# Kernel tuning notes

Measured on AMD Instinct MI355X. Metric: run time of the kernel, lower is better.

## Reference

```python
import jax, jax.numpy as jnp
import numpy as np

E, HEADS, HD, L, FF = 768, 12, 64, 12, 3072


def layernorm(x, g, b, eps=1e-5):
    m = jnp.mean(x, axis=-1, keepdims=True)
    v = jnp.var(x, axis=-1, keepdims=True)
    return (x - m) / jnp.sqrt(v + eps) * g + b


def setup_inputs() -> dict:
    key = jax.random.key(0)
    ks = jax.random.split(key, 26)
    B, N, PS = 32, 1024, 24
    P2 = PS * PS
    def rn(k, shape, s=0.02):
        return jax.random.normal(k, shape, dtype=jnp.float32) * s
    return {
        "scene_masks": jax.random.normal(ks[0], (B, N, PS, PS), dtype=jnp.float32),
        "target_mask": jax.random.normal(ks[1], (B, PS, PS), dtype=jnp.float32),
        "emb_W": rn(ks[2], (E, P2)),            # torch Linear weight [out,in]
        "emb_b": rn(ks[3], (E,)),
        "class_embed": rn(ks[4], (1, 1, E)),
        "scene_pos": rn(ks[5], (1, N + 1, E)),
        "target_pos": rn(ks[6], (1, 2, E)),
        "ln1_g": jnp.ones((L, E), jnp.float32),
        "ln1_b": jnp.zeros((L, E), jnp.float32),
        "ln2_g": jnp.ones((L, E), jnp.float32),
        "ln2_b": jnp.zeros((L, E), jnp.float32),
        "Wq": rn(ks[7], (L, HD, HD)),
        "Wk": rn(ks[8], (L, HD, HD)),
        "Wv": rn(ks[9], (L, HD, HD)),
        "Wo": rn(ks[10], (L, E, E)),
        "bo": rn(ks[11], (L, E)),
        "W1": rn(ks[12], (L, FF, E)),
        "b1": rn(ks[13], (L, FF)),
        "W2": rn(ks[14], (L, E, FF)),
        "b2": rn(ks[15], (L, E)),
        "mlp_W": rn(ks[16], (N, E)),
        "mlp_b": rn(ks[17], (N,)),
    }


def _forward_logits(scene_masks, target_mask, emb_W, emb_b, class_embed, scene_pos,
                    target_pos, ln1_g, ln1_b, ln2_g, ln2_b, Wq, Wk, Wv, Wo, bo,
                    W1, b1, W2, b2, mlp_W, mlp_b):
    B, N, H, W = scene_masks.shape
    P2 = H * W
    scene = scene_masks.reshape(B, N, P2) @ emb_W.T + emb_b          # [B,N,E]
    tgt = target_mask.reshape(B, 1, P2) @ emb_W.T + emb_b            # [B,1,E]
    cls = jnp.broadcast_to(class_embed, (B, 1, E))
    scene = jnp.concatenate([cls, scene], axis=1) + scene_pos[:, :N + 1]  # [B,N+1,E]
    tgt = jnp.concatenate([cls, tgt], axis=1) + target_pos               # [B,2,E]
    scale = jnp.sqrt(jnp.float32(E))

    def block(tq, p):
        g1, bb1n, g2, bb2n, wq, wk, wv, wo, bo_, w1, b1_, w2, b2_ = p
        kv = layernorm(scene, g1, bb1n)                # norm1(value)=norm1(key)
        q = layernorm(tq, g1, bb1n)                    # norm1(query)
        kvh = kv.reshape(B, N + 1, HEADS, HD)
        qh = q.reshape(B, 2, HEADS, HD)
        # per-head Linear shares one [HD,HD] weight across all heads
        qs = jnp.einsum('nqhd,ed->nqhe', qh, wq)
        ks_ = jnp.einsum('nkhd,ed->nkhe', kvh, wk)
        vs = jnp.einsum('nkhd,ed->nkhe', kvh, wv)
        energy = jnp.einsum('nqhd,nkhd->nhqk', qs, ks_)     # [B,H,2,N+1]
        att = jax.nn.softmax(energy / scale, axis=-1)
        out = jnp.einsum('nhqk,nkhd->nqhd', att, vs).reshape(B, 2, E)
        out = out @ wo.T + bo_
        x = layernorm(out + tq, g1, bb1n)
        ff = jax.nn.relu(x @ w1.T + b1_) @ w2.T + b2_
        return layernorm(ff + x, g2, bb2n), None

    params = (ln1_g, ln1_b, ln2_g, ln2_b, Wq, Wk, Wv, Wo, bo, W1, b1, W2, b2)
    tgt, _ = jax.lax.scan(block, tgt, params)
    x = jnp.mean(tgt, axis=1) @ mlp_W.T + mlp_b       # [B, num_patches]
    return x


def reference(scene_masks, target_mask, emb_W, emb_b, class_embed, scene_pos,
              target_pos, ln1_g, ln1_b, ln2_g, ln2_b, Wq, Wk, Wv, Wo, bo,
              W1, b1, W2, b2, mlp_W, mlp_b):
    x = _forward_logits(scene_masks, target_mask, emb_W, emb_b, class_embed,
                        scene_pos, target_pos, ln1_g, ln1_b, ln2_g, ln2_b,
                        Wq, Wk, Wv, Wo, bo, W1, b1, W2, b2, mlp_W, mlp_b)
    # sorted_nodes = argsort desc + 1; eye(P+1)[nodes-1] == one_hot(argsort desc)
    order = jnp.argsort(-x, axis=1)[:, :5]                # top-5 patch indices
    return jax.nn.one_hot(order, x.shape[1] + 1, dtype=jnp.float32)  # [B,5,P+1]
```

## Files before the change

kernel.cpp:

```cpp
#include <hip/hip_runtime.h>
#include <math.h>

#define E_DIM 768
#define NTOK 1025
#define B_DIM 32
#define NHEADS 12
#define HDIM 64
#define LAYERS 12
#define FF_DIM 3072
#define P2 576

__device__ __forceinline__ float block_reduce_sum(float v, float* red) {
  int tid = threadIdx.x;
  red[tid] = v;
  __syncthreads();
#pragma unroll
  for (int s = 128; s > 0; s >>= 1) {
    if (tid < s) red[tid] += red[tid + s];
    __syncthreads();
  }
  float r = red[0];
  __syncthreads();
  return r;
}

__global__ __launch_bounds__(256) void embed_gemm(
    const float* __restrict__ A, const float* __restrict__ W,
    const float* __restrict__ bias, const float* __restrict__ pos,
    float* __restrict__ scene) {
  __shared__ float Xs[16][132];
  __shared__ float Ws[16][132];
  int tid = threadIdx.x;
  int n0 = blockIdx.x * 128;
  int m0 = blockIdx.y * 128;
  int lr = tid >> 2;
  int lk = (tid & 3) << 2;
  int ty = tid >> 4, tx = tid & 15;
  float acc[8][8] = {};
  for (int k0 = 0; k0 < P2; k0 += 16) {
    float4 x0 = *(const float4*)(A + (size_t)(m0 + lr) * P2 + k0 + lk);
    float4 x1 = *(const float4*)(A + (size_t)(m0 + 64 + lr) * P2 + k0 + lk);
    float4 w0 = *(const float4*)(W + (size_t)(n0 + lr) * P2 + k0 + lk);
    float4 w1 = *(const float4*)(W + (size_t)(n0 + 64 + lr) * P2 + k0 + lk);
    __syncthreads();
    Xs[lk + 0][lr] = x0.x; Xs[lk + 1][lr] = x0.y; Xs[lk + 2][lr] = x0.z; Xs[lk + 3][lr] = x0.w;
    Xs[lk + 0][64 + lr] = x1.x; Xs[lk + 1][64 + lr] = x1.y; Xs[lk + 2][64 + lr] = x1.z; Xs[lk + 3][64 + lr] = x1.w;
    Ws[lk + 0][lr] = w0.x; Ws[lk + 1][lr] = w0.y; Ws[lk + 2][lr] = w0.z; Ws[lk + 3][lr] = w0.w;
    Ws[lk + 0][64 + lr] = w1.x; Ws[lk + 1][64 + lr] = w1.y; Ws[lk + 2][64 + lr] = w1.z; Ws[lk + 3][64 + lr] = w1.w;
    __syncthreads();
#pragma unroll
    for (int kk = 0; kk < 16; ++kk) {
      float4 a0 = *(const float4*)&Xs[kk][ty << 2];
      float4 a1 = *(const float4*)&Xs[kk][64 + (ty << 2)];
      float4 b0 = *(const float4*)&Ws[kk][tx << 2];
      float4 b1 = *(const float4*)&Ws[kk][64 + (tx << 2)];
      float av[8] = {a0.x, a0.y, a0.z, a0.w, a1.x, a1.y, a1.z, a1.w};
      float bv[8] = {b0.x, b0.y, b0.z, b0.w, b1.x, b1.y, b1.z, b1.w};
#pragma unroll
      for (int i = 0; i < 8; ++i)
#pragma unroll
        for (int j = 0; j < 8; ++j) acc[i][j] += av[i] * bv[j];
    }
  }
#pragma unroll
  for (int i = 0; i < 8; ++i) {
    int mloc = (i < 4) ? ((ty << 2) + i) : (64 + (ty << 2) + i - 4);
    int m = m0 + mloc;
    int b = m >> 10, nt = m & 1023;
    size_t row = ((size_t)b * NTOK + 1 + nt) * E_DIM;
    size_t prow = (size_t)(1 + nt) * E_DIM;
#pragma unroll
    for (int half = 0; half < 2; ++half) {
      int n = n0 + half * 64 + (tx << 2);
      float4 o4;
      o4.x = acc[i][half * 4 + 0] + bias[n + 0] + pos[prow + n + 0];
      o4.y = acc[i][half * 4 + 1] + bias[n + 1] + pos[prow + n + 1];
      o4.z = acc[i][half * 4 + 2] + bias[n + 2] + pos[prow + n + 2];
      o4.w = acc[i][half * 4 + 3] + bias[n + 3] + pos[prow + n + 3];
      *(float4*)&scene[row + n] = o4;
    }
  }
}

__global__ void scene_cls(const float* __restrict__ cls, const float* __restrict__ pos,
                          float* __restrict__ scene) {
  int b = blockIdx.x;
  for (int e = threadIdx.x; e < E_DIM; e += 256)
    scene[(size_t)b * NTOK * E_DIM + e] = cls[e] + pos[e];
}

__global__ __launch_bounds__(256) void ln_rows(const float* __restrict__ in, float* __restrict__ out) {
  __shared__ float red[256];
  int r = blockIdx.x, tid = threadIdx.x;
  const float* x = in + (size_t)r * E_DIM;
  float a0 = x[tid], a1 = x[tid + 256], a2 = x[tid + 512];
  float mean = block_reduce_sum(a0 + a1 + a2, red) * (1.f / 768.f);
  float d0 = a0 - mean, d1 = a1 - mean, d2 = a2 - mean;
  float var = block_reduce_sum(d0 * d0 + d1 * d1 + d2 * d2, red) * (1.f / 768.f);
  float rinv = rsqrtf(var + 1e-5f);
  float* o = out + (size_t)r * E_DIM;
  o[tid] = d0 * rinv; o[tid + 256] = d1 * rinv; o[tid + 512] = d2 * rinv;
}

__global__ __launch_bounds__(256) void tgt_init(
    const float* __restrict__ tmask, const float* __restrict__ W,
    const float* __restrict__ bias, const float* __restrict__ cls,
    const float* __restrict__ tpos, float* __restrict__ tq) {
  int b = blockIdx.x, tid = threadIdx.x;
  for (int e = tid; e < E_DIM; e += 256)
    tq[(size_t)(b * 2) * E_DIM + e] = cls[e] + tpos[e];
  const float* tm = tmask + (size_t)b * P2;
  for (int e = tid; e < E_DIM; e += 256) {
    const float* wr = W + (size_t)e * P2;
    float s = 0.f;
    for (int k = 0; k < P2; k += 4) {
      float4 w4 = *(const float4*)&wr[k];
      float4 t4 = *(const float4*)&tm[k];
      s += w4.x * t4.x + w4.y * t4.y + w4.z * t4.z + w4.w * t4.w;
    }
    tq[(size_t)(b * 2 + 1) * E_DIM + e] = s + bias[e] + tpos[E_DIM + e];
  }
}

__global__ void prep_m(const float* __restrict__ Wq, const float* __restrict__ Wk,
                       float* __restrict__ Mb) {
  int l = blockIdx.y;
  int idx = blockIdx.x * 256 + threadIdx.x;
  int d = idx >> 6, dp = idx & 63;
  const float* wq = Wq + l * 4096;
  const float* wk = Wk + l * 4096;
  float s = 0.f;
#pragma unroll 8
  for (int e = 0; e < 64; ++e) s += wq[e * 64 + d] * wk[e * 64 + dp];
  Mb[l * 4096 + idx] = s;
}

__global__ void prep_wvo(const float* __restrict__ Wv, const float* __restrict__ Wo,
                         float* __restrict__ Wvo) {
  int l = blockIdx.y;
  int idx = blockIdx.x * 256 + threadIdx.x;
  int ep = idx / 768, hd = idx % 768;
  int h = hd >> 6, d = hd & 63;
  const float* wv = Wv + (size_t)l * 4096;
  const float* wo = Wo + (size_t)l * 768 * 768 + (size_t)ep * 768 + h * 64;
  float s = 0.f;
#pragma unroll 8
  for (int ev = 0; ev < 64; ++ev) s += wv[ev * 64 + d] * wo[ev];
  Wvo[(size_t)l * 589824 + idx] = s;
}

__global__ __launch_bounds__(256) void qln_qm(
    const float* __restrict__ tq, const float* __restrict__ g1,
    const float* __restrict__ b1, const float* __restrict__ Mb, int l,
    float* __restrict__ qMg, float* __restrict__ qMb) {
  __shared__ float q[768];
  __shared__ float qm[768];
  __shared__ float red[256];
  int r = blockIdx.x, tid = threadIdx.x;
  const float* x = tq + (size_t)r * E_DIM;
  float a0 = x[tid], a1 = x[tid + 256], a2 = x[tid + 512];
  float mean = block_reduce_sum(a0 + a1 + a2, red) * (1.f / 768.f);
  float d0 = a0 - mean, d1 = a1 - mean, d2 = a2 - mean;
  float var = block_reduce_sum(d0 * d0 + d1 * d1 + d2 * d2, red) * (1.f / 768.f);
  float rinv = rsqrtf(var + 1e-5f);
  const float* gl = g1 + l * E_DIM;
  const float* bl = b1 + l * E_DIM;
  q[tid] = d0 * rinv * gl[tid] + bl[tid];
  q[tid + 256] = d1 * rinv * gl[tid + 256] + bl[tid + 256];
  q[tid + 512] = d2 * rinv * gl[tid + 512] + bl[tid + 512];
  __syncthreads();
  const float* M = Mb + l * 4096;
  const float inv_scale = rsqrtf(768.f);
  for (int o = tid; o < 768; o += 256) {
    int h = o >> 6, dp = o & 63;
    const float* qh = q + h * 64;
    float s = 0.f;
#pragma unroll 8
    for (int d = 0; d < 64; ++d) s += qh[d] * M[d * 64 + dp];
    qm[o] = s;
    qMg[(size_t)r * E_DIM + o] = s * gl[o] * inv_scale;
  }
  __syncthreads();
  if (tid < NHEADS) {
    float acc = 0.f;
#pragma unroll 8
    for (int dp = 0; dp < 64; ++dp) acc += qm[tid * 64 + dp] * bl[tid * 64 + dp];
    qMb[r * NHEADS + tid] = acc * inv_scale;
  }
}

#define ACH 272
__global__ __launch_bounds__(256) void attn_flash(
    const float* __restrict__ ns, const float* __restrict__ qMg,
    const float* __restrict__ qMb, const float* __restrict__ g1,
    const float* __restrict__ b1, int l, float* __restrict__ ctx) {
  __shared__ float red[256];
  __shared__ float sred[2][16];
  __shared__ float cred[2][16][64];
  int b = blockIdx.x / NHEADS;
  int h = blockIdx.x % NHEADS;
  int tid = threadIdx.x;
  int g = tid >> 4;
  int lane = tid & 15;
  int r0 = b * 2, r1 = r0 + 1;
  const float* nsb = ns + (size_t)b * NTOK * E_DIM + h * 64;
  float4 q0v = *(const float4*)(qMg + (size_t)r0 * E_DIM + h * 64 + lane * 4);
  float4 q1v = *(const float4*)(qMg + (size_t)r1 * E_DIM + h * 64 + lane * 4);
  float qb0 = qMb[r0 * NHEADS + h], qb1 = qMb[r1 * NHEADS + h];
  float m = -1e30f, s0 = 0.f, s1 = 0.f;
  float4 c0 = {0, 0, 0, 0}, c1 = {0, 0, 0, 0};
  float4 v[17];
  float e0a[17], e1a[17];
  for (int cb = 0; cb < NTOK; cb += ACH) {
    int ntk = NTOK - cb; if (ntk > ACH) ntk = ACH;
    int cnt = (ntk - g + 15) >> 4;
    float mloc = -1e30f;
#pragma unroll
    for (int i = 0; i < 17; ++i) {
      if (i < cnt) {
        int k = cb + g + (i << 4);
        float4 vv = *(const float4*)(nsb + (size_t)k * E_DIM + lane * 4);
        v[i] = vv;
        float p0 = vv.x * q0v.x + vv.y * q0v.y + vv.z * q0v.z + vv.w * q0v.w;
        float p1 = vv.x * q1v.x + vv.y * q1v.y + vv.z * q1v.z + vv.w * q1v.w;
#pragma unroll
        for (int off = 8; off; off >>= 1) {
          p0 += __shfl_xor(p0, off, 16);
          p1 += __shfl_xor(p1, off, 16);
        }
        float e0 = p0 + qb0, e1 = p1 + qb1;
        e0a[i] = e0; e1a[i] = e1;
        mloc = fmaxf(mloc, fmaxf(e0, e1));
      }
    }
    red[tid] = mloc;
    __syncthreads();
#pragma unroll
    for (int s = 128; s > 0; s >>= 1) {
      if (tid < s) red[tid] = fmaxf(red[tid], red[tid + s]);
      __syncthreads();
    }
    float mnew = fmaxf(m, red[0]);
    __syncthreads();
    if (mnew > m) {
      float f = expf(m - mnew);
      s0 *= f; s1 *= f;
      c0.x *= f; c0.y *= f; c0.z *= f; c0.w *= f;
      c1.x *= f; c1.y *= f; c1.z *= f; c1.w *= f;
      m = mnew;
    }
#pragma unroll
    for (int i = 0; i < 17; ++i) {
      if (i < cnt) {
        float p0 = expf(e0a[i] - m);
        float p1 = expf(e1a[i] - m);
        s0 += p0; s1 += p1;
        c0.x += p0 * v[i].x; c0.y += p0 * v[i].y; c0.z += p0 * v[i].z; c0.w += p0 * v[i].w;
        c1.x += p1 * v[i].x; c1.y += p1 * v[i].y; c1.z += p1 * v[i].z; c1.w += p1 * v[i].w;
      }
    }
  }
  if (lane == 0) { sred[0][g] = s0; sred[1][g] = s1; }
  *(float4*)&cred[0][g][lane * 4] = c0;
  *(float4*)&cred[1][g][lane * 4] = c1;
  __syncthreads();
  if (tid < 128) {
    int t = tid >> 6, d = tid & 63;
    float stot = 0.f, cs = 0.f;
#pragma unroll
    for (int gg = 0; gg < 16; ++gg) { stot += sred[t][gg]; cs += cred[t][gg][d]; }
    float inv = 1.f / stot;
    int o = h * 64 + d;
    ctx[(size_t)(r0 + t) * E_DIM + o] = cs * inv * g1[l * E_DIM + o] + b1[l * E_DIM + o];
  }
}

__global__ __launch_bounds__(256) void skinny_part(
    const float* __restrict__ X, int K, const float* __restrict__ W,
    int kchunk, float* __restrict__ part, int N) {
  __shared__ float Xs[16][64];
  __shared__ float Ws[16][64];
  int tid = threadIdx.x;
  int n0 = blockIdx.x * 64;
  int s = blockIdx.y;
  int kbeg = s * kchunk;
  int lr = tid >> 2;
  int lk = (tid & 3) << 2;
  int ty = tid >> 4, tx = tid & 15;
  float acc[4][4] = {};
  for (int k0 = kbeg; k0 < kbeg + kchunk; k0 += 16) {
    float4 xv = *(const float4*)(X + (size_t)lr * K + k0 + lk);
    float4 wv = *(const float4*)(W + (size_t)(n0 + lr) * K + k0 + lk);
    __syncthreads();
    Xs[lk + 0][lr] = xv.x; Xs[lk + 1][lr] = xv.y; Xs[lk + 2][lr] = xv.z; Xs[lk + 3][lr] = xv.w;
    Ws[lk + 0][lr] = wv.x; Ws[lk + 1][lr] = wv.y; Ws[lk + 2][lr] = wv.z; Ws[lk + 3][lr] = wv.w;
    __syncthreads();
#pragma unroll
    for (int kk = 0; kk < 16; ++kk) {
      float4 a4 = *(const float4*)&Xs[kk][ty << 2];
      float4 b4 = *(const float4*)&Ws[kk][tx << 2];
      float av[4] = {a4.x, a4.y, a4.z, a4.w};
      float bv[4] = {b4.x, b4.y, b4.z, b4.w};
#pragma unroll
      for (int i = 0; i < 4; ++i)
#pragma unroll
        for (int j = 0; j < 4; ++j) acc[i][j] += av[i] * bv[j];
    }
  }
#pragma unroll
  for (int i = 0; i < 4; ++i) {
    int mm = (ty << 2) + i;
    float4 o4 = make_float4(acc[i][0], acc[i][1], acc[i][2], acc[i][3]);
    *(float4*)&part[((size_t)s * 64 + mm) * N + n0 + (tx << 2)] = o4;
  }
}

__global__ __launch_bounds__(256) void reduce_bias(
    const float* __restrict__ part, int S, int N,
    const float* __restrict__ bias, int relu, float* __restrict__ out) {
  int m = blockIdx.x;
  for (int n = threadIdx.x; n < N; n += 256) {
    float s = 0.f;
    for (int i = 0; i < S; ++i) s += part[((size_t)i * 64 + m) * N + n];
    s += bias[n];
    if (relu) s = fmaxf(s, 0.f);
    out[(size_t)m * N + n] = s;
  }
}

__global__ __launch_bounds__(256) void reduce_ln_q(
    const float* __restrict__ part, int S, const float* __restrict__ bias,
    const float* __restrict__ res, const float* __restrict__ g,
    const float* __restrict__ bsh, float* __restrict__ out,
    const float* __restrict__ Mb_next, const float* __restrict__ g1n,
    const float* __restrict__ b1n, float* __restrict__ qMg,
    float* __restrict__ qMb) {
  __shared__ float red[256];
  __shared__ float q[768];
  __shared__ float qm[768];
  int m = blockIdx.x, tid = threadIdx.x;
  float t[3];
#pragma unroll
  for (int c = 0; c < 3; ++c) {
    int n = tid + c * 256;
    float s = 0.f;
    for (int i = 0; i < S; ++i) s += part[((size_t)i * 64 + m) * 768 + n];
    t[c] = s + bias[n] + res[(size_t)m * 768 + n];
  }
  float mean = block_reduce_sum(t[0] + t[1] + t[2], red) * (1.f / 768.f);
  float d0 = t[0] - mean, d1 = t[1] - mean, d2 = t[2] - mean;
  float var = block_reduce_sum(d0 * d0 + d1 * d1 + d2 * d2, red) * (1.f / 768.f);
  float rinv = rsqrtf(var + 1e-5f);
  float y0 = d0 * rinv * g[tid] + bsh[tid];
  float y1 = d1 * rinv * g[tid + 256] + bsh[tid + 256];
  float y2 = d2 * rinv * g[tid + 512] + bsh[tid + 512];
  out[(size_t)m * 768 + tid] = y0;
  out[(size_t)m * 768 + tid + 256] = y1;
  out[(size_t)m * 768 + tid + 512] = y2;
  if (Mb_next) {
    float mean2 = block_reduce_sum(y0 + y1 + y2, red) * (1.f / 768.f);
    float e0 = y0 - mean2, e1 = y1 - mean2, e2 = y2 - mean2;
    float var2 = block_reduce_sum(e0 * e0 + e1 * e1 + e2 * e2, red) * (1.f / 768.f);
    float rinv2 = rsqrtf(var2 + 1e-5f);
    q[tid] = e0 * rinv2 * g1n[tid] + b1n[tid];
    q[tid + 256] = e1 * rinv2 * g1n[tid + 256] + b1n[tid + 256];
    q[tid + 512] = e2 * rinv2 * g1n[tid + 512] + b1n[tid + 512];
    __syncthreads();
    const float inv_scale = rsqrtf(768.f);
    for (int o = tid; o < 768; o += 256) {
      int h = o >> 6, dp = o & 63;
      const float* qh = q + h * 64;
      float s = 0.f;
#pragma unroll 8
      for (int d = 0; d < 64; ++d) s += qh[d] * Mb_next[d * 64 + dp];
      qm[o] = s;
      qMg[(size_t)m * E_DIM + o] = s * g1n[o] * inv_scale;
    }
    __syncthreads();
    if (tid < NHEADS) {
      float acc = 0.f;
#pragma unroll 8
      for (int dp = 0; dp < 64; ++dp) acc += qm[tid * 64 + dp] * b1n[tid * 64 + dp];
      qMb[m * NHEADS + tid] = acc * inv_scale;
    }
  }
}

__global__ void mean_rows(const float* __restrict__ tq, float* __restrict__ xm) {
  int idx = blockIdx.x * 256 + threadIdx.x;
  int b = idx / E_DIM, e = idx % E_DIM;
  xm[idx] = (b < 32)
      ? 0.5f * (tq[(size_t)(b * 2) * E_DIM + e] + tq[(size_t)(b * 2 + 1) * E_DIM + e])
      : 0.f;
}

__global__ __launch_bounds__(256) void top5_onehot(const float* __restrict__ logits,
                                                   float* __restrict__ out) {
  __shared__ float v[1024];
  __shared__ float bv[256];
  __shared__ int bi[256];
  int b = blockIdx.x, tid = threadIdx.x;
  for (int i = tid; i < 1024; i += 256) v[i] = logits[(size_t)b * 1024 + i];
  float* ob = out + (size_t)b * 5 * NTOK;
  for (int i = tid; i < 5 * NTOK; i += 256) ob[i] = 0.f;
  __syncthreads();
  for (int it = 0; it < 5; ++it) {
    float best = -1e38f;
    int bidx = 0x7fffffff;
    for (int i = tid; i < 1024; i += 256) {
      float x = v[i];
      if (x > best || (x == best && i < bidx)) { best = x; bidx = i; }
    }
    bv[tid] = best; bi[tid] = bidx;
    __syncthreads();
    for (int s = 128; s > 0; s >>= 1) {
      if (tid < s) {
        if (bv[tid + s] > bv[tid] || (bv[tid + s] == bv[tid] && bi[tid + s] < bi[tid])) {
          bv[tid] = bv[tid + s]; bi[tid] = bi[tid + s];
        }
      }
      __syncthreads();
    }
    if (tid == 0) {
      ob[it * NTOK + bi[0]] = 1.0f;
      v[bi[0]] = -1e38f;
    }
    __syncthreads();
  }
}

extern "C" void kernel_launch(void* const* d_in, const int* in_sizes, int n_in,
                              void* d_out, int out_size, void* d_ws, size_t ws_size,
                              hipStream_t stream) {
  const float* scene_masks = (const float*)d_in[0];
  const float* target_mask = (const float*)d_in[1];
  const float* emb_W = (const float*)d_in[2];
  const float* emb_b = (const float*)d_in[3];
  const float* class_embed = (const float*)d_in[4];
  const float* scene_pos = (const float*)d_in[5];
  const float* target_pos = (const float*)d_in[6];
  const float* ln1_g = (const float*)d_in[7];
  const float* ln1_b = (const float*)d_in[8];
  const float* ln2_g = (const float*)d_in[9];
  const float* ln2_b = (const float*)d_in[10];
  const float* Wq = (const float*)d_in[11];
  const float* Wk = (const float*)d_in[12];
  const float* Wv = (const float*)d_in[13];
  const float* Wo = (const float*)d_in[14];
  const float* bo = (const float*)d_in[15];
  const float* W1 = (const float*)d_in[16];
  const float* fb1 = (const float*)d_in[17];
  const float* W2 = (const float*)d_in[18];
  const float* fb2 = (const float*)d_in[19];
  const float* mlp_W = (const float*)d_in[20];
  const float* mlp_b = (const float*)d_in[21];
  float* out = (float*)d_out;

  float* ws = (float*)d_ws;
  float* scene = ws;
  float* Mbuf = scene + 25190400;
  float* Wvo = Mbuf + 49152;
  float* tq = Wvo + 7077888;
  float* qMg = tq + 49152;
  float* qMb = qMg + 49152;
  float* ctxf = qMb + 768;
  float* xbuf = ctxf + 49152;
  float* h1 = xbuf + 49152;
  float* xm = h1 + 196608;
  float* logits = xm + 49152;
  float* part = logits + 65536;

  embed_gemm<<<dim3(6, 256), 256, 0, stream>>>(scene_masks, emb_W, emb_b, scene_pos, scene);
  scene_cls<<<32, 256, 0, stream>>>(class_embed, scene_pos, scene);
  ln_rows<<<32 * NTOK, 256, 0, stream>>>(scene, scene);
  tgt_init<<<32, 256, 0, stream>>>(target_mask, emb_W, emb_b, class_embed, target_pos, tq);
  prep_m<<<dim3(16, 12), 256, 0, stream>>>(Wq, Wk, Mbuf);
  prep_wvo<<<dim3(2304, 12), 256, 0, stream>>>(Wv, Wo, Wvo);
  qln_qm<<<64, 256, 0, stream>>>(tq, ln1_g, ln1_b, Mbuf, 0, qMg, qMb);

  for (int l = 0; l < LAYERS; ++l) {
    attn_flash<<<32 * NHEADS, 256, 0, stream>>>(scene, qMg, qMb, ln1_g, ln1_b, l, ctxf);
    skinny_part<<<dim3(12, 8), 256, 0, stream>>>(ctxf, 768, Wvo + (size_t)l * 589824, 96, part, 768);
    reduce_ln_q<<<64, 256, 0, stream>>>(part, 8, bo + l * 768, tq,
                                        ln1_g + l * 768, ln1_b + l * 768, xbuf,
                                        nullptr, nullptr, nullptr, nullptr, nullptr);
    skinny_part<<<dim3(48, 4), 256, 0, stream>>>(xbuf, 768, W1 + (size_t)l * FF_DIM * 768, 192, part, FF_DIM);
    reduce_bias<<<64, 256, 0, stream>>>(part, 4, FF_DIM, fb1 + l * FF_DIM, 1, h1);
    skinny_part<<<dim3(12, 16), 256, 0, stream>>>(h1, FF_DIM, W2 + (size_t)l * 768 * FF_DIM, 192, part, 768);
    if (l < LAYERS - 1) {
      reduce_ln_q<<<64, 256, 0, stream>>>(part, 16, fb2 + l * 768, xbuf,
                                          ln2_g + l * 768, ln2_b + l * 768, tq,
                                          Mbuf + (l + 1) * 4096, ln1_g + (l + 1) * 768,
                                          ln1_b + (l + 1) * 768, qMg, qMb);
    } else {
      reduce_ln_q<<<64, 256, 0, stream>>>(part, 16, fb2 + l * 768, xbuf,
                                          ln2_g + l * 768, ln2_b + l * 768, tq,
                                          nullptr, nullptr, nullptr, nullptr, nullptr);
    }
  }

  mean_rows<<<192, 256, 0, stream>>>(tq, xm);
  skinny_part<<<dim3(16, 4), 256, 0, stream>>>(xm, 768, mlp_W, 192, part, 1024);
  reduce_bias<<<64, 256, 0, stream>>>(part, 4, 1024, mlp_b, 0, logits);
  top5_onehot<<<32, 256, 0, stream>>>(logits, out);
}
```

Measured before the change: 2.088 ms.

## Fuse per-layer transformer loop into persistent megakernel with grid barriers

Replaces the per-layer launch sequence (attention, three skinny GEMMs, reductions, plus the final head) with one persistent kernel of 384 blocks that runs each stage in turn, separated by software grid barriers built on atomics. The goal is to remove roughly a hundred kernel launches and their gaps. Split-K factors also change (Wvo 8→4 splits, W2 stays 16) and the mean over target rows is now accumulated with atomics during the last layernorm. The cost is barrier spin overhead, many idle blocks in the small stages, and a deadlock risk if all 384 blocks are not co-resident; the barrier's timeout break would then silently go on with wrong data.

```diff
diff --git a/kernel.cpp b/kernel.cpp
--- a/kernel.cpp
+++ b/kernel.cpp
@@ -9,6 +9,7 @@
 #define LAYERS 12
 #define FF_DIM 3072
 #define P2 576
+#define GRID 384
 
 __device__ __forceinline__ float block_reduce_sum(float v, float* red) {
   int tid = threadIdx.x;
@@ -22,6 +23,21 @@
   float r = red[0];
   __syncthreads();
   return r;
+}
+
+__device__ __forceinline__ void grid_barrier(unsigned* cnt, unsigned target) {
+  __syncthreads();
+  if (threadIdx.x == 0) {
+    __threadfence();
+    atomicAdd(cnt, 1u);
+    unsigned it = 0;
+    while (atomicAdd(cnt, 0u) < target) {
+      if (++it > 200000u) break;
+      __builtin_amdgcn_s_sleep(2);
+    }
+    __threadfence();
+  }
+  __syncthreads();
 }
 
 __global__ __launch_bounds__(256) void embed_gemm(
@@ -149,56 +165,56 @@
   Wvo[(size_t)l * 589824 + idx] = s;
 }
 
-__global__ __launch_bounds__(256) void qln_qm(
-    const float* __restrict__ tq, const float* __restrict__ g1,
-    const float* __restrict__ b1, const float* __restrict__ Mb, int l,
-    float* __restrict__ qMg, float* __restrict__ qMb) {
-  __shared__ float q[768];
-  __shared__ float qm[768];
-  __shared__ float red[256];
-  int r = blockIdx.x, tid = threadIdx.x;
-  const float* x = tq + (size_t)r * E_DIM;
-  float a0 = x[tid], a1 = x[tid + 256], a2 = x[tid + 512];
-  float mean = block_reduce_sum(a0 + a1 + a2, red) * (1.f / 768.f);
-  float d0 = a0 - mean, d1 = a1 - mean, d2 = a2 - mean;
-  float var = block_reduce_sum(d0 * d0 + d1 * d1 + d2 * d2, red) * (1.f / 768.f);
-  float rinv = rsqrtf(var + 1e-5f);
-  const float* gl = g1 + l * E_DIM;
-  const float* bl = b1 + l * E_DIM;
-  q[tid] = d0 * rinv * gl[tid] + bl[tid];
-  q[tid + 256] = d1 * rinv * gl[tid + 256] + bl[tid + 256];
-  q[tid + 512] = d2 * rinv * gl[tid + 512] + bl[tid + 512];
-  __syncthreads();
-  const float* M = Mb + l * 4096;
+struct GemmS { float Xs[16][64]; float Ws[16][64]; };
+struct AttnS { float red[256]; float sred[2][16]; float cred[2][16][64]; };
+struct LnS   { float red[256]; float q[768]; float qm[768]; };
+struct TopS  { float v[1024]; float bv[256]; int bi[256]; };
+
+__device__ void dev_qproj(LnS& L, int m, const float* gl, const float* bl,
+                          const float* M, float* qMg, float* qMb) {
+  int tid = threadIdx.x;
   const float inv_scale = rsqrtf(768.f);
   for (int o = tid; o < 768; o += 256) {
     int h = o >> 6, dp = o & 63;
-    const float* qh = q + h * 64;
+    const float* qh = L.q + h * 64;
     float s = 0.f;
 #pragma unroll 8
     for (int d = 0; d < 64; ++d) s += qh[d] * M[d * 64 + dp];
-    qm[o] = s;
-    qMg[(size_t)r * E_DIM + o] = s * gl[o] * inv_scale;
+    L.qm[o] = s;
+    qMg[(size_t)m * E_DIM + o] = s * gl[o] * inv_scale;
   }
   __syncthreads();
   if (tid < NHEADS) {
     float acc = 0.f;
 #pragma unroll 8
-    for (int dp = 0; dp < 64; ++dp) acc += qm[tid * 64 + dp] * bl[tid * 64 + dp];
-    qMb[r * NHEADS + tid] = acc * inv_scale;
-  }
+    for (int dp = 0; dp < 64; ++dp) acc += L.qm[tid * 64 + dp] * bl[tid * 64 + dp];
+    qMb[m * NHEADS + tid] = acc * inv_scale;
+  }
+}
+
+__device__ void dev_qln0(LnS& L, int m, const float* tq, const float* g1,
+                         const float* b1, const float* Mb, float* qMg, float* qMb) {
+  int tid = threadIdx.x;
+  const float* x = tq + (size_t)m * E_DIM;
+  float a0 = x[tid], a1 = x[tid + 256], a2 = x[tid + 512];
+  float mean = block_reduce_sum(a0 + a1 + a2, L.red) * (1.f / 768.f);
+  float d0 = a0 - mean, d1 = a1 - mean, d2 = a2 - mean;
+  float var = block_reduce_sum(d0 * d0 + d1 * d1 + d2 * d2, L.red) * (1.f / 768.f);
+  float rinv = rsqrtf(var + 1e-5f);
+  L.q[tid] = d0 * rinv * g1[tid] + b1[tid];
+  L.q[tid + 256] = d1 * rinv * g1[tid + 256] + b1[tid + 256];
+  L.q[tid + 512] = d2 * rinv * g1[tid + 512] + b1[tid + 512];
+  __syncthreads();
+  dev_qproj(L, m, g1, b1, Mb, qMg, qMb);
 }
 
 #define ACH 272
-__global__ __launch_bounds__(256) void attn_flash(
-    const float* __restrict__ ns, const float* __restrict__ qMg,
-    const float* __restrict__ qMb, const float* __restrict__ g1,
-    const float* __restrict__ b1, int l, float* __restrict__ ctx) {
-  __shared__ float red[256];
-  __shared__ float sred[2][16];
-  __shared__ float cred[2][16][64];
-  int b = blockIdx.x / NHEADS;
-  int h = blockIdx.x % NHEADS;
+__device__ void dev_attn(AttnS& A, const float* __restrict__ ns,
+                         const float* __restrict__ qMg, const float* __restrict__ qMb,
+                         const float* __restrict__ g1, const float* __restrict__ b1,
+                         int l, float* __restrict__ ctx, int bid) {
+  int b = bid / NHEADS;
+  int h = bid % NHEADS;
   int tid = threadIdx.x;
   int g = tid >> 4;
   int lane = tid & 15;
@@ -233,14 +249,14 @@
         mloc = fmaxf(mloc, fmaxf(e0, e1));
       }
     }
-    red[tid] = mloc;
+    A.red[tid] = mloc;
     __syncthreads();
 #pragma unroll
     for (int s = 128; s > 0; s >>= 1) {
-      if (tid < s) red[tid] = fmaxf(red[tid], red[tid + s]);
+      if (tid < s) A.red[tid] = fmaxf(A.red[tid], A.red[tid + s]);
       __syncthreads();
     }
-    float mnew = fmaxf(m, red[0]);
+    float mnew = fmaxf(m, A.red[0]);
     __syncthreads();
     if (mnew > m) {
       float f = expf(m - mnew);
@@ -260,29 +276,24 @@
       }
     }
   }
-  if (lane == 0) { sred[0][g] = s0; sred[1][g] = s1; }
-  *(float4*)&cred[0][g][lane * 4] = c0;
-  *(float4*)&cred[1][g][lane * 4] = c1;
+  if (lane == 0) { A.sred[0][g] = s0; A.sred[1][g] = s1; }
+  *(float4*)&A.cred[0][g][lane * 4] = c0;
+  *(float4*)&A.cred[1][g][lane * 4] = c1;
   __syncthreads();
   if (tid < 128) {
-    int t = tid >> 6, d = tid & 63;
+    int t = tid >> 6, dd = tid & 63;
+    int o = h * 64 + dd;
     float stot = 0.f, cs = 0.f;
 #pragma unroll
-    for (int gg = 0; gg < 16; ++gg) { stot += sred[t][gg]; cs += cred[t][gg][d]; }
+    for (int gg = 0; gg < 16; ++gg) { stot += A.sred[t][gg]; cs += A.cred[t][gg][dd]; }
     float inv = 1.f / stot;
-    int o = h * 64 + d;
     ctx[(size_t)(r0 + t) * E_DIM + o] = cs * inv * g1[l * E_DIM + o] + b1[l * E_DIM + o];
   }
 }
 
-__global__ __launch_bounds__(256) void skinny_part(
-    const float* __restrict__ X, int K, const float* __restrict__ W,
-    int kchunk, float* __restrict__ part, int N) {
-  __shared__ float Xs[16][64];
-  __shared__ float Ws[16][64];
-  int tid = threadIdx.x;
-  int n0 = blockIdx.x * 64;
-  int s = blockIdx.y;
+__device__ void dev_skinny(GemmS& G, const float* X, int K, const float* W,
+                           int kchunk, float* part, int N, int n0, int s) {
+  int tid = threadIdx.x;
   int kbeg = s * kchunk;
   int lr = tid >> 2;
   int lk = (tid & 3) << 2;
@@ -292,13 +303,13 @@
     float4 xv = *(const float4*)(X + (size_t)lr * K + k0 + lk);
     float4 wv = *(const float4*)(W + (size_t)(n0 + lr) * K + k0 + lk);
     __syncthreads();
-    Xs[lk + 0][lr] = xv.x; Xs[lk + 1][lr] = xv.y; Xs[lk + 2][lr] = xv.z; Xs[lk + 3][lr] = xv.w;
-    Ws[lk + 0][lr] = wv.x; Ws[lk + 1][lr] = wv.y; Ws[lk + 2][lr] = wv.z; Ws[lk + 3][lr] = wv.w;
+    G.Xs[lk + 0][lr] = xv.x; G.Xs[lk + 1][lr] = xv.y; G.Xs[lk + 2][lr] = xv.z; G.Xs[lk + 3][lr] = xv.w;
+    G.Ws[lk + 0][lr] = wv.x; G.Ws[lk + 1][lr] = wv.y; G.Ws[lk + 2][lr] = wv.z; G.Ws[lk + 3][lr] = wv.w;
     __syncthreads();
 #pragma unroll
     for (int kk = 0; kk < 16; ++kk) {
-      float4 a4 = *(const float4*)&Xs[kk][ty << 2];
-      float4 b4 = *(const float4*)&Ws[kk][tx << 2];
+      float4 a4 = *(const float4*)&G.Xs[kk][ty << 2];
+      float4 b4 = *(const float4*)&G.Ws[kk][tx << 2];
       float av[4] = {a4.x, a4.y, a4.z, a4.w};
       float bv[4] = {b4.x, b4.y, b4.z, b4.w};
 #pragma unroll
@@ -315,10 +326,8 @@
   }
 }
 
-__global__ __launch_bounds__(256) void reduce_bias(
-    const float* __restrict__ part, int S, int N,
-    const float* __restrict__ bias, int relu, float* __restrict__ out) {
-  int m = blockIdx.x;
+__device__ void dev_reduce_bias(const float* part, int S, int N,
+                                const float* bias, int relu, float* out, int m) {
   for (int n = threadIdx.x; n < N; n += 256) {
     float s = 0.f;
     for (int i = 0; i < S; ++i) s += part[((size_t)i * 64 + m) * N + n];
@@ -328,17 +337,12 @@
   }
 }
 
-__global__ __launch_bounds__(256) void reduce_ln_q(
-    const float* __restrict__ part, int S, const float* __restrict__ bias,
-    const float* __restrict__ res, const float* __restrict__ g,
-    const float* __restrict__ bsh, float* __restrict__ out,
-    const float* __restrict__ Mb_next, const float* __restrict__ g1n,
-    const float* __restrict__ b1n, float* __restrict__ qMg,
-    float* __restrict__ qMb) {
-  __shared__ float red[256];
-  __shared__ float q[768];
-  __shared__ float qm[768];
-  int m = blockIdx.x, tid = threadIdx.x;
+__device__ void dev_reduce_ln_q(LnS& L, const float* part, int S, const float* bias,
+                                const float* res, const float* g, const float* bsh,
+                                float* out, const float* Mb_next, const float* g1n,
+                                const float* b1n, float* qMg, float* qMb,
+                                float* xmean, int m) {
+  int tid = threadIdx.x;
   float t[3];
 #pragma unroll
   for (int c = 0; c < 3; ++c) {
@@ -347,9 +351,9 @@
     for (int i = 0; i < S; ++i) s += part[((size_t)i * 64 + m) * 768 + n];
     t[c] = s + bias[n] + res[(size_t)m * 768 + n];
   }
-  float mean = block_reduce_sum(t[0] + t[1] + t[2], red) * (1.f / 768.f);
+  float mean = block_reduce_sum(t[0] + t[1] + t[2], L.red) * (1.f / 768.f);
   float d0 = t[0] - mean, d1 = t[1] - mean, d2 = t[2] - mean;
-  float var = block_reduce_sum(d0 * d0 + d1 * d1 + d2 * d2, red) * (1.f / 768.f);
+  float var = block_reduce_sum(d0 * d0 + d1 * d1 + d2 * d2, L.red) * (1.f / 768.f);
   float rinv = rsqrtf(var + 1e-5f);
   float y0 = d0 * rinv * g[tid] + bsh[tid];
   float y1 = d1 * rinv * g[tid + 256] + bsh[tid + 256];
@@ -357,50 +361,33 @@
   out[(size_t)m * 768 + tid] = y0;
   out[(size_t)m * 768 + tid + 256] = y1;
   out[(size_t)m * 768 + tid + 512] = y2;
+  if (xmean) {
+    float* xr = xmean + (size_t)(m >> 1) * 768;
+    atomicAdd(&xr[tid], 0.5f * y0);
+    atomicAdd(&xr[tid + 256], 0.5f * y1);
+    atomicAdd(&xr[tid + 512], 0.5f * y2);
+  }
   if (Mb_next) {
-    float mean2 = block_reduce_sum(y0 + y1 + y2, red) * (1.f / 768.f);
+    float mean2 = block_reduce_sum(y0 + y1 + y2, L.red) * (1.f / 768.f);
     float e0 = y0 - mean2, e1 = y1 - mean2, e2 = y2 - mean2;
-    float var2 = block_reduce_sum(e0 * e0 + e1 * e1 + e2 * e2, red) * (1.f / 768.f);
+    float var2 = block_reduce_sum(e0 * e0 + e1 * e1 + e2 * e2, L.red) * (1.f / 768.f);
     float rinv2 = rsqrtf(var2 + 1e-5f);
-    q[tid] = e0 * rinv2 * g1n[tid] + b1n[tid];
-    q[tid + 256] = e1 * rinv2 * g1n[tid + 256] + b1n[tid + 256];
-    q[tid + 512] = e2 * rinv2 * g1n[tid + 512] + b1n[tid + 512];
-    __syncthreads();
-    const float inv_scale = rsqrtf(768.f);
-    for (int o = tid; o < 768; o += 256) {
-      int h = o >> 6, dp = o & 63;
-      const float* qh = q + h * 64;
-      float s = 0.f;
-#pragma unroll 8
-      for (int d = 0; d < 64; ++d) s += qh[d] * Mb_next[d * 64 + dp];
-      qm[o] = s;
-      qMg[(size_t)m * E_DIM + o] = s * g1n[o] * inv_scale;
-    }
-    __syncthreads();
-    if (tid < NHEADS) {
-      float acc = 0.f;
-#pragma unroll 8
-      for (int dp = 0; dp < 64; ++dp) acc += qm[tid * 64 + dp] * b1n[tid * 64 + dp];
-      qMb[m * NHEADS + tid] = acc * inv_scale;
-    }
-  }
-}
-
-__global__ void mean_rows(const float* __restrict__ tq, float* __restrict__ xm) {
-  int idx = blockIdx.x * 256 + threadIdx.x;
-  int b = idx / E_DIM, e = idx % E_DIM;
-  xm[idx] = (b < 32)
-      ? 0.5f * (tq[(size_t)(b * 2) * E_DIM + e] + tq[(size_t)(b * 2 + 1) * E_DIM + e])
-      : 0.f;
-}
-
-__global__ __launch_bounds__(256) void top5_onehot(const float* __restrict__ logits,
-                                                   float* __restrict__ out) {
-  __shared__ float v[1024];
-  __shared__ float bv[256];
-  __shared__ int bi[256];
-  int b = blockIdx.x, tid = threadIdx.x;
-  for (int i = tid; i < 1024; i += 256) v[i] = logits[(size_t)b * 1024 + i];
+    L.q[tid] = e0 * rinv2 * g1n[tid] + b1n[tid];
+    L.q[tid + 256] = e1 * rinv2 * g1n[tid + 256] + b1n[tid + 256];
+    L.q[tid + 512] = e2 * rinv2 * g1n[tid + 512] + b1n[tid + 512];
+    __syncthreads();
+    dev_qproj(L, m, g1n, b1n, Mb_next, qMg, qMb);
+  }
+}
+
+__device__ void dev_top5(TopS& T, const float* part, const float* bias,
+                         float* out, int b) {
+  int tid = threadIdx.x;
+  for (int i = tid; i < 1024; i += 256) {
+    float s = part[(size_t)(0 * 64 + b) * 1024 + i] + part[(size_t)(1 * 64 + b) * 1024 + i] +
+              part[(size_t)(2 * 64 + b) * 1024 + i] + part[(size_t)(3 * 64 + b) * 1024 + i];
+    T.v[i] = s + bias[i];
+  }
   float* ob = out + (size_t)b * 5 * NTOK;
   for (int i = tid; i < 5 * NTOK; i += 256) ob[i] = 0.f;
   __syncthreads();
@@ -408,25 +395,96 @@
     float best = -1e38f;
     int bidx = 0x7fffffff;
     for (int i = tid; i < 1024; i += 256) {
-      float x = v[i];
+      float x = T.v[i];
       if (x > best || (x == best && i < bidx)) { best = x; bidx = i; }
     }
-    bv[tid] = best; bi[tid] = bidx;
+    T.bv[tid] = best; T.bi[tid] = bidx;
     __syncthreads();
     for (int s = 128; s > 0; s >>= 1) {
       if (tid < s) {
-        if (bv[tid + s] > bv[tid] || (bv[tid + s] == bv[tid] && bi[tid + s] < bi[tid])) {
-          bv[tid] = bv[tid + s]; bi[tid] = bi[tid + s];
+        if (T.bv[tid + s] > T.bv[tid] ||
+            (T.bv[tid + s] == T.bv[tid] && T.bi[tid + s] < T.bi[tid])) {
+          T.bv[tid] = T.bv[tid + s]; T.bi[tid] = T.bi[tid + s];
         }
       }
       __syncthreads();
     }
     if (tid == 0) {
-      ob[it * NTOK + bi[0]] = 1.0f;
-      v[bi[0]] = -1e38f;
-    }
-    __syncthreads();
-  }
+      ob[it * NTOK + T.bi[0]] = 1.0f;
+      T.v[T.bi[0]] = -1e38f;
+    }
+    __syncthreads();
+  }
+}
+
+struct MegaArgs {
+  const float* scene;
+  const float* Mbuf; const float* Wvo;
+  const float* ln1_g; const float* ln1_b; const float* ln2_g; const float* ln2_b;
+  const float* bo; const float* W1; const float* fb1; const float* W2; const float* fb2;
+  const float* mlp_W; const float* mlp_b;
+  float* tq; float* qMg; float* qMb; float* ctx; float* xbuf; float* h1;
+  float* xm; float* partA; float* partB; float* out;
+  unsigned* cnt;
+};
+
+__global__ __launch_bounds__(256, 2) void mega(MegaArgs P) {
+  __shared__ __align__(16) float smem_raw[2432];
+  GemmS& G = *(GemmS*)smem_raw;
+  AttnS& A = *(AttnS*)smem_raw;
+  LnS& L = *(LnS*)smem_raw;
+  TopS& T = *(TopS*)smem_raw;
+  int bid = blockIdx.x;
+  unsigned gen = 0;
+#define GBAR() do { ++gen; grid_barrier(P.cnt, gen * (unsigned)GRID); } while (0)
+
+  if (bid < 64)
+    dev_qln0(L, bid, P.tq, P.ln1_g, P.ln1_b, P.Mbuf, P.qMg, P.qMb);
+  GBAR();
+
+  for (int l = 0; l < LAYERS; ++l) {
+    dev_attn(A, P.scene, P.qMg, P.qMb, P.ln1_g, P.ln1_b, l, P.ctx, bid);
+    GBAR();
+    if (bid < 48)
+      dev_skinny(G, P.ctx, 768, P.Wvo + (size_t)l * 589824, 192, P.partA, 768,
+                 (bid % 12) * 64, bid / 12);
+    GBAR();
+    if (bid < 64)
+      dev_reduce_ln_q(L, P.partA, 4, P.bo + l * 768, P.tq,
+                      P.ln1_g + l * 768, P.ln1_b + l * 768, P.xbuf,
+                      nullptr, nullptr, nullptr, nullptr, nullptr, nullptr, bid);
+    GBAR();
+    if (bid < 192)
+      dev_skinny(G, P.xbuf, 768, P.W1 + (size_t)l * FF_DIM * 768, 192, P.partB,
+                 FF_DIM, (bid % 48) * 64, bid / 48);
+    GBAR();
+    if (bid < 64)
+      dev_reduce_bias(P.partB, 4, FF_DIM, P.fb1 + l * FF_DIM, 1, P.h1, bid);
+    GBAR();
+    if (bid < 192)
+      dev_skinny(G, P.h1, FF_DIM, P.W2 + (size_t)l * 768 * FF_DIM, 192, P.partA,
+                 768, (bid % 12) * 64, bid / 12);
+    GBAR();
+    if (bid < 64) {
+      if (l < LAYERS - 1)
+        dev_reduce_ln_q(L, P.partA, 16, P.fb2 + l * 768, P.xbuf,
+                        P.ln2_g + l * 768, P.ln2_b + l * 768, P.tq,
+                        P.Mbuf + (l + 1) * 4096, P.ln1_g + (l + 1) * 768,
+                        P.ln1_b + (l + 1) * 768, P.qMg, P.qMb, nullptr, bid);
+      else
+        dev_reduce_ln_q(L, P.partA, 16, P.fb2 + l * 768, P.xbuf,
+                        P.ln2_g + l * 768, P.ln2_b + l * 768, P.tq,
+                        nullptr, nullptr, nullptr, nullptr, nullptr, P.xm, bid);
+    }
+    GBAR();
+  }
+
+  if (bid < 64)
+    dev_skinny(G, P.xm, 768, P.mlp_W, 192, P.partA, 1024, (bid % 16) * 64, bid / 16);
+  GBAR();
+  if (bid < 32)
+    dev_top5(T, P.partA, P.mlp_b, P.out, bid);
+#undef GBAR
 }
 
 extern "C" void kernel_launch(void* const* d_in, const int* in_sizes, int n_in,
@@ -467,8 +525,9 @@
   float* xbuf = ctxf + 49152;
   float* h1 = xbuf + 49152;
   float* xm = h1 + 196608;
-  float* logits = xm + 49152;
-  float* part = logits + 65536;
+  float* partA = xm + 49152;
+  float* partB = partA + 786432;
+  unsigned* cnt = (unsigned*)(partB + 786432);
 
   embed_gemm<<<dim3(6, 256), 256, 0, stream>>>(scene_masks, emb_W, emb_b, scene_pos, scene);
   scene_cls<<<32, 256, 0, stream>>>(class_embed, scene_pos, scene);
@@ -476,31 +535,17 @@
   tgt_init<<<32, 256, 0, stream>>>(target_mask, emb_W, emb_b, class_embed, target_pos, tq);
   prep_m<<<dim3(16, 12), 256, 0, stream>>>(Wq, Wk, Mbuf);
   prep_wvo<<<dim3(2304, 12), 256, 0, stream>>>(Wv, Wo, Wvo);
-  qln_qm<<<64, 256, 0, stream>>>(tq, ln1_g, ln1_b, Mbuf, 0, qMg, qMb);
-
-  for (int l = 0; l < LAYERS; ++l) {
-    attn_flash<<<32 * NHEADS, 256, 0, stream>>>(scene, qMg, qMb, ln1_g, ln1_b, l, ctxf);
-    skinny_part<<<dim3(12, 8), 256, 0, stream>>>(ctxf, 768, Wvo + (size_t)l * 589824, 96, part, 768);
-    reduce_ln_q<<<64, 256, 0, stream>>>(part, 8, bo + l * 768, tq,
-                                        ln1_g + l * 768, ln1_b + l * 768, xbuf,
-                                        nullptr, nullptr, nullptr, nullptr, nullptr);
-    skinny_part<<<dim3(48, 4), 256, 0, stream>>>(xbuf, 768, W1 + (size_t)l * FF_DIM * 768, 192, part, FF_DIM);
-    reduce_bias<<<64, 256, 0, stream>>>(part, 4, FF_DIM, fb1 + l * FF_DIM, 1, h1);
-    skinny_part<<<dim3(12, 16), 256, 0, stream>>>(h1, FF_DIM, W2 + (size_t)l * 768 * FF_DIM, 192, part, 768);
-    if (l < LAYERS - 1) {
-      reduce_ln_q<<<64, 256, 0, stream>>>(part, 16, fb2 + l * 768, xbuf,
-                                          ln2_g + l * 768, ln2_b + l * 768, tq,
-                                          Mbuf + (l + 1) * 4096, ln1_g + (l + 1) * 768,
-                                          ln1_b + (l + 1) * 768, qMg, qMb);
-    } else {
-      reduce_ln_q<<<64, 256, 0, stream>>>(part, 16, fb2 + l * 768, xbuf,
-                                          ln2_g + l * 768, ln2_b + l * 768, tq,
-                                          nullptr, nullptr, nullptr, nullptr, nullptr);
-    }
-  }
-
-  mean_rows<<<192, 256, 0, stream>>>(tq, xm);
-  skinny_part<<<dim3(16, 4), 256, 0, stream>>>(xm, 768, mlp_W, 192, part, 1024);
-  reduce_bias<<<64, 256, 0, stream>>>(part, 4, 1024, mlp_b, 0, logits);
-  top5_onehot<<<32, 256, 0, stream>>>(logits, out);
-}
+  hipMemsetAsync(xm, 0, 49152 * sizeof(float), stream);
+  hipMemsetAsync(cnt, 0, 256 * sizeof(unsigned), stream);
+
+  MegaArgs ma;
+  ma.scene = scene;
+  ma.Mbuf = Mbuf; ma.Wvo = Wvo;
+  ma.ln1_g = ln1_g; ma.ln1_b = ln1_b; ma.ln2_g = ln2_g; ma.ln2_b = ln2_b;
+  ma.bo = bo; ma.W1 = W1; ma.fb1 = fb1; ma.W2 = W2; ma.fb2 = fb2;
+  ma.mlp_W = mlp_W; ma.mlp_b = mlp_b;
+  ma.tq = tq; ma.qMg = qMg; ma.qMb = qMb; ma.ctx = ctxf; ma.xbuf = xbuf;
+  ma.h1 = h1; ma.xm = xm; ma.partA = partA; ma.partB = partB; ma.out = out;
+  ma.cnt = cnt;
+  mega<<<GRID, 256, 0, stream>>>(ma);
+}
```

Result: slower. 5.059 ms (+142.3%).
